# Optimization experiments

Hardware: AMD Instinct MI355X
Metric: run time of the kernel (lower is better)

The kernel has to match this reference:

```python
import jax, jax.numpy as jnp
import numpy as np

EPS_NORM = 1e-6  # MVLayerNorm epsilon


def _build_cayley():
    # Cl(3,0): blades as bitmasks, ordered by (grade, bitmask):
    # [1, e1, e2, e3, e12, e13, e23, e123]
    n = 3
    order = sorted(range(1 << n), key=lambda b: (bin(b).count('1'), b))
    idx = {b: i for i, b in enumerate(order)}
    C = np.zeros((8, 8, 8), dtype=np.float32)
    for a in range(8):
        for b in range(8):
            # sign from reordering basis vectors (Euclidean metric: e_i^2 = +1)
            swaps, ash = 0, a >> 1
            while ash:
                swaps += bin(ash & b).count('1')
                ash >>= 1
            C[idx[a], idx[a ^ b], idx[b]] = -1.0 if swaps % 2 else 1.0
    return C

_CAYLEY_NP = _build_cayley()
CAYLEY = jnp.asarray(_CAYLEY_NP)
# metric of each blade: scalar part of blade*blade -> [1,1,1,1,-1,-1,-1,-1]
METRIC = jnp.asarray(np.array([_CAYLEY_NP[i, 0, i] for i in range(8)], dtype=np.float32))
# blade -> grade subspace index, subspace dims [1,3,3,1]
BLADE2SUB = np.array([0, 1, 1, 1, 2, 2, 2, 3])


def mv_linear(x, w, b):
    # x: (B, in, 8); w: (out, in, 4); b: (out,) added to scalar blade only
    wb = w[:, :, BLADE2SUB]                      # (out, in, 8) per-blade weight
    y = jnp.einsum('bmi,nmi->bni', x, wb)        # (B, out, 8)
    return y.at[..., 0].add(b)


def mv_layernorm(x, a):
    # quadratic form per channel: q = sum_i g_i * x_i^2, shape (B, C, 1)
    q = jnp.einsum('bci,i,bci->bc', x, METRIC, x)[..., None]
    norm = (q * q + 1e-16) ** 0.25               # smooth sqrt(|q|)
    norm = norm.mean(axis=1, keepdims=True) + EPS_NORM  # (B, 1, 1)
    return a[None, :, None] * x / norm


def setup_inputs() -> dict:
    key = jax.random.key(0)
    ks = jax.random.split(key, 8)
    N, C_IN, C_HID, NSUB = 4096, 512, 512, 4
    s = 1.0 / np.sqrt(C_IN)
    return {
        'x': jax.random.normal(ks[0], (N, C_IN, 8), jnp.float32),
        'w1': jax.random.normal(ks[1], (C_HID, C_IN, NSUB), jnp.float32) * s,
        'b1': jax.random.normal(ks[2], (C_HID,), jnp.float32) * 0.02,
        'w2': jax.random.normal(ks[3], (C_HID, C_IN, NSUB), jnp.float32) * s,
        'b2': jax.random.normal(ks[4], (C_HID,), jnp.float32) * 0.02,
        'w3': jax.random.normal(ks[5], (C_IN, C_HID, NSUB), jnp.float32) * s,
        'b3': jax.random.normal(ks[6], (C_IN,), jnp.float32) * 0.02,
        'a_norm': jax.random.normal(ks[7], (C_IN,), jnp.float32) * 0.1 + 1.0,
    }


def reference(x, w1, b1, w2, b2, w3, b3, a_norm):
    x_l = mv_linear(x, w1, b1)                       # (N, hid, 8)
    x_r = mv_linear(x, w2, b2)                       # (N, hid, 8)
    gp = jnp.einsum('bni,ijk,bnk->bnj', x_l, CAYLEY, x_r)  # sparse Cayley product
    y = mv_linear(gp, w3, b3)                        # (N, in, 8)
    return mv_layernorm(y, a_norm)
```

## Files before the change

kernel.cpp:

```cpp
#include <hip/hip_runtime.h>
#include <hip/hip_bf16.h>
#include <cstdint>
#include <cstddef>

typedef __bf16 bf16;
typedef __bf16 bf16x2_t __attribute__((ext_vector_type(2)));
typedef __bf16 bf16x4_t __attribute__((ext_vector_type(4)));
typedef __bf16 bf16x8_t __attribute__((ext_vector_type(8)));
typedef float  f32x2_t  __attribute__((ext_vector_type(2)));
typedef float  f32x4_t  __attribute__((ext_vector_type(4)));

#define NTOK 4096
#define CH   512
#define SLICE (NTOK*CH)
#define WSLICE (CH*CH)

#define AS1 __attribute__((address_space(1)))
#define AS3 __attribute__((address_space(3)))

__device__ __forceinline__ void gl_lds16(const void* g, void* l) {
    __builtin_amdgcn_global_load_lds((const AS1 unsigned int*)g,
                                     (AS3 unsigned int*)l, 16, 0, 0);
}

__global__ __launch_bounds__(256) void k_convert_x(const float* __restrict__ x,
                                                   bf16* __restrict__ xb) {
    int p = blockIdx.x * 256 + threadIdx.x;
    const f32x4_t* x4 = (const f32x4_t*)x;
    f32x4_t v0 = x4[2*p];
    f32x4_t v1 = x4[2*p+1];
    xb[0*SLICE + p] = (bf16)v0.x;
    xb[1*SLICE + p] = (bf16)v0.y;
    xb[2*SLICE + p] = (bf16)v0.z;
    xb[3*SLICE + p] = (bf16)v0.w;
    xb[4*SLICE + p] = (bf16)v1.x;
    xb[5*SLICE + p] = (bf16)v1.y;
    xb[6*SLICE + p] = (bf16)v1.z;
    xb[7*SLICE + p] = (bf16)v1.w;
}

__global__ __launch_bounds__(256) void k_convert_w(const float* __restrict__ w1,
                                                   const float* __restrict__ w2,
                                                   const float* __restrict__ w3,
                                                   bf16* __restrict__ w1b,
                                                   bf16* __restrict__ w2b,
                                                   bf16* __restrict__ w3b) {
    int p = blockIdx.x * 256 + threadIdx.x;
    const float* w = (blockIdx.y == 0) ? w1 : (blockIdx.y == 1) ? w2 : w3;
    bf16* wb       = (blockIdx.y == 0) ? w1b : (blockIdx.y == 1) ? w2b : w3b;
    f32x4_t v = ((const f32x4_t*)w)[p];
    wb[0*WSLICE + p] = (bf16)v.x;
    wb[1*WSLICE + p] = (bf16)v.y;
    wb[2*WSLICE + p] = (bf16)v.z;
    wb[3*WSLICE + p] = (bf16)v.w;
}

__global__ __launch_bounds__(512, 2) void k_gemm12(const bf16* __restrict__ xb,
                                                   const bf16* __restrict__ w1b,
                                                   const bf16* __restrict__ w2b,
                                                   bf16* __restrict__ xl,
                                                   bf16* __restrict__ xr) {
    const int blade = blockIdx.z;
    const int sub = (blade == 0) ? 0 : (blade < 4) ? 1 : (blade < 7) ? 2 : 3;
    const bf16* A  = xb  + (size_t)blade * SLICE;
    const bf16* B1 = w1b + (size_t)sub * WSLICE;
    const bf16* B2 = w2b + (size_t)sub * WSLICE;
    const int tm = blockIdx.x * 256, tn = blockIdx.y * 128;

    __shared__ __align__(1024) bf16 lsA[2][256 * 64];
    __shared__ __align__(1024) bf16 lsB1[2][128 * 64];
    __shared__ __align__(1024) bf16 lsB2[2][128 * 64];

    const int t = threadIdx.x, lane = t & 63, wid = t >> 6;
    const int waveM = (wid >> 2) * 128, waveN = (wid & 3) * 32;

    const int srow = t >> 3;
    const int sswz = ((t & 7) ^ (srow & 7)) * 8;
    const bf16* Ag  = A  + (size_t)(tm + srow) * CH + sswz;
    const bf16* B1g = B1 + (size_t)(tn + srow) * CH + sswz;
    const bf16* B2g = B2 + (size_t)(tn + srow) * CH + sswz;
    const int wbase = wid * 1024;

    const int xorv  = (lane & 7) << 4;
    const int kbase = (lane >> 4) * 16;

    f32x4_t accL[8][2] = {};
    f32x4_t accR[8][2] = {};

    {
        char* la  = (char*)lsA[0]  + wbase;
        char* lb1 = (char*)lsB1[0] + wbase;
        char* lb2 = (char*)lsB2[0] + wbase;
        #pragma unroll
        for (int q = 0; q < 4; ++q)
            gl_lds16(Ag + (size_t)q * 64 * CH, la + q * 8192);
        #pragma unroll
        for (int q = 0; q < 2; ++q) {
            gl_lds16(B1g + (size_t)q * 64 * CH, lb1 + q * 8192);
            gl_lds16(B2g + (size_t)q * 64 * CH, lb2 + q * 8192);
        }
    }

    #pragma unroll 2
    for (int kt = 0; kt < 8; ++kt) {
        const int cur = kt & 1;
        __syncthreads();
        if (kt < 7) {
            const int k0 = (kt + 1) * 64;
            char* la  = (char*)lsA[cur ^ 1]  + wbase;
            char* lb1 = (char*)lsB1[cur ^ 1] + wbase;
            char* lb2 = (char*)lsB2[cur ^ 1] + wbase;
            #pragma unroll
            for (int q = 0; q < 4; ++q)
                gl_lds16(Ag + (size_t)q * 64 * CH + k0, la + q * 8192);
            #pragma unroll
            for (int q = 0; q < 2; ++q) {
                gl_lds16(B1g + (size_t)q * 64 * CH + k0, lb1 + q * 8192);
                gl_lds16(B2g + (size_t)q * 64 * CH + k0, lb2 + q * 8192);
            }
        }
        const char* ca  = (const char*)lsA[cur];
        const char* cb1 = (const char*)lsB1[cur];
        const char* cb2 = (const char*)lsB2[cur];
        #pragma unroll
        for (int kk = 0; kk < 2; ++kk) {
            const int koff = kk * 64 + kbase;
            bf16x8_t af[8], b1f[2], b2f[2];
            #pragma unroll
            for (int mf = 0; mf < 8; ++mf) {
                int row = waveM + mf * 16 + (lane & 15);
                af[mf] = *(const bf16x8_t*)(ca + row * 128 + (koff ^ xorv));
            }
            #pragma unroll
            for (int nf = 0; nf < 2; ++nf) {
                int row = waveN + nf * 16 + (lane & 15);
                b1f[nf] = *(const bf16x8_t*)(cb1 + row * 128 + (koff ^ xorv));
                b2f[nf] = *(const bf16x8_t*)(cb2 + row * 128 + (koff ^ xorv));
            }
            __builtin_amdgcn_s_setprio(1);
            #pragma unroll
            for (int mf = 0; mf < 8; ++mf)
                #pragma unroll
                for (int nf = 0; nf < 2; ++nf) {
                    accL[mf][nf] = __builtin_amdgcn_mfma_f32_16x16x32_bf16(
                        af[mf], b1f[nf], accL[mf][nf], 0, 0, 0);
                    accR[mf][nf] = __builtin_amdgcn_mfma_f32_16x16x32_bf16(
                        af[mf], b2f[nf], accR[mf][nf], 0, 0, 0);
                }
            __builtin_amdgcn_s_setprio(0);
        }
    }

    bf16* O1 = xl + (size_t)blade * SLICE;
    bf16* O2 = xr + (size_t)blade * SLICE;
    const int orow0 = tm + waveM + (lane >> 4) * 4;
    const int ocol  = tn + waveN + (lane & 15);
    #pragma unroll
    for (int mf = 0; mf < 8; ++mf)
        #pragma unroll
        for (int r = 0; r < 4; ++r) {
            size_t rowoff = (size_t)(orow0 + mf * 16 + r) * CH;
            #pragma unroll
            for (int nf = 0; nf < 2; ++nf) {
                O1[rowoff + ocol + nf * 16] = (bf16)accL[mf][nf][r];
                O2[rowoff + ocol + nf * 16] = (bf16)accR[mf][nf][r];
            }
        }
}

__global__ __launch_bounds__(512, 2) void k_gemm3(const bf16* __restrict__ gp,
                                                  const bf16* __restrict__ w3b,
                                                  bf16* __restrict__ yb) {
    const int blade = blockIdx.z;
    const int sub = (blade == 0) ? 0 : (blade < 4) ? 1 : (blade < 7) ? 2 : 3;
    const bf16* A = gp  + (size_t)blade * SLICE;
    const bf16* B = w3b + (size_t)sub * WSLICE;
    const int tm = blockIdx.x * 256, tn = blockIdx.y * 256;

    __shared__ __align__(1024) bf16 lsA[2][256 * 64];
    __shared__ __align__(1024) bf16 lsB[2][256 * 64];

    const int t = threadIdx.x, lane = t & 63, wid = t >> 6;
    const int waveM = (wid >> 2) * 128, waveN = (wid & 3) * 64;

    const int srow = t >> 3;
    const int sswz = ((t & 7) ^ (srow & 7)) * 8;
    const bf16* Ag = A + (size_t)(tm + srow) * CH + sswz;
    const bf16* Bg = B + (size_t)(tn + srow) * CH + sswz;
    const int wbase = wid * 1024;

    const int xorv  = (lane & 7) << 4;
    const int kbase = (lane >> 4) * 16;

    f32x4_t acc[8][4] = {};

    {
        char* la = (char*)lsA[0] + wbase;
        char* lb = (char*)lsB[0] + wbase;
        #pragma unroll
        for (int q = 0; q < 4; ++q) {
            gl_lds16(Ag + (size_t)q * 64 * CH, la + q * 8192);
            gl_lds16(Bg + (size_t)q * 64 * CH, lb + q * 8192);
        }
    }

    #pragma unroll 2
    for (int kt = 0; kt < 8; ++kt) {
        const int cur = kt & 1;
        __syncthreads();
        if (kt < 7) {
            const int k0 = (kt + 1) * 64;
            char* la = (char*)lsA[cur ^ 1] + wbase;
            char* lb = (char*)lsB[cur ^ 1] + wbase;
            #pragma unroll
            for (int q = 0; q < 4; ++q) {
                gl_lds16(Ag + (size_t)q * 64 * CH + k0, la + q * 8192);
                gl_lds16(Bg + (size_t)q * 64 * CH + k0, lb + q * 8192);
            }
        }
        const char* ca = (const char*)lsA[cur];
        const char* cb = (const char*)lsB[cur];
        #pragma unroll
        for (int kk = 0; kk < 2; ++kk) {
            const int koff = kk * 64 + kbase;
            bf16x8_t af[8], bf[4];
            #pragma unroll
            for (int mf = 0; mf < 8; ++mf) {
                int row = waveM + mf * 16 + (lane & 15);
                af[mf] = *(const bf16x8_t*)(ca + row * 128 + (koff ^ xorv));
            }
            #pragma unroll
            for (int nf = 0; nf < 4; ++nf) {
                int row = waveN + nf * 16 + (lane & 15);
                bf[nf] = *(const bf16x8_t*)(cb + row * 128 + (koff ^ xorv));
            }
            __builtin_amdgcn_s_setprio(1);
            #pragma unroll
            for (int mf = 0; mf < 8; ++mf)
                #pragma unroll
                for (int nf = 0; nf < 4; ++nf)
                    acc[mf][nf] = __builtin_amdgcn_mfma_f32_16x16x32_bf16(
                        af[mf], bf[nf], acc[mf][nf], 0, 0, 0);
            __builtin_amdgcn_s_setprio(0);
        }
    }

    bf16* O = yb + (size_t)blade * SLICE;
    const int orow0 = tm + waveM + (lane >> 4) * 4;
    const int ocol  = tn + waveN + (lane & 15);
    #pragma unroll
    for (int mf = 0; mf < 8; ++mf)
        #pragma unroll
        for (int r = 0; r < 4; ++r) {
            size_t rowoff = (size_t)(orow0 + mf * 16 + r) * CH;
            #pragma unroll
            for (int nf = 0; nf < 4; ++nf)
                O[rowoff + ocol + nf * 16] = (bf16)acc[mf][nf][r];
        }
}

__global__ __launch_bounds__(256) void k_gp(const bf16* __restrict__ xl,
                                            const bf16* __restrict__ xr,
                                            const float* __restrict__ b1,
                                            const float* __restrict__ b2,
                                            bf16* __restrict__ gp) {
    int p = (blockIdx.x * 256 + threadIdx.x) * 4;
    float l[8][4], r[8][4], g[8][4];
    #pragma unroll
    for (int i = 0; i < 8; ++i) {
        bf16x4_t lv = *(const bf16x4_t*)(xl + (size_t)i * SLICE + p);
        bf16x4_t rv = *(const bf16x4_t*)(xr + (size_t)i * SLICE + p);
        #pragma unroll
        for (int v = 0; v < 4; ++v) { l[i][v] = (float)lv[v]; r[i][v] = (float)rv[v]; g[i][v] = 0.f; }
    }
    int n0 = p & (CH - 1);
    f32x4_t b1v = *(const f32x4_t*)(b1 + n0);
    f32x4_t b2v = *(const f32x4_t*)(b2 + n0);
    #pragma unroll
    for (int v = 0; v < 4; ++v) { l[0][v] += b1v[v]; r[0][v] += b2v[v]; }

    const int IDX[8] = {0, 1, 2, 4, 3, 5, 6, 7};
    #pragma unroll
    for (int a = 0; a < 8; ++a) {
        #pragma unroll
        for (int b = 0; b < 8; ++b) {
            int e = ((((a >> 1) ^ (a >> 2)) & b) & 1) ^ (((a >> 2) & (b >> 1)) & 1);
            int j = IDX[a ^ b], ia = IDX[a], ib = IDX[b];
            #pragma unroll
            for (int v = 0; v < 4; ++v)
                g[j][v] += e ? (-l[ia][v] * r[ib][v]) : (l[ia][v] * r[ib][v]);
        }
    }
    #pragma unroll
    for (int i = 0; i < 8; ++i) {
        bf16x4_t gv;
        #pragma unroll
        for (int v = 0; v < 4; ++v) gv[v] = (bf16)g[i][v];
        *(bf16x4_t*)(gp + (size_t)i * SLICE + p) = gv;
    }
}

__global__ __launch_bounds__(256) void k_ln(const bf16* __restrict__ y,
                                            const float* __restrict__ b3,
                                            const float* __restrict__ an,
                                            float* __restrict__ out) {
    int b = blockIdx.x, t = threadIdx.x;
    int c0 = t * 2;
    size_t base = (size_t)b * CH + c0;
    float yv[2][8];
    #pragma unroll
    for (int i = 0; i < 8; ++i) {
        bf16x2_t v = *(const bf16x2_t*)(y + (size_t)i * SLICE + base);
        yv[0][i] = (float)v[0];
        yv[1][i] = (float)v[1];
    }
    f32x2_t b3v = *(const f32x2_t*)(b3 + c0);
    float nsum = 0.f;
    #pragma unroll
    for (int h = 0; h < 2; ++h) {
        yv[h][0] += b3v[h];
        float q = yv[h][0]*yv[h][0] + yv[h][1]*yv[h][1] + yv[h][2]*yv[h][2] + yv[h][3]*yv[h][3]
                - yv[h][4]*yv[h][4] - yv[h][5]*yv[h][5] - yv[h][6]*yv[h][6] - yv[h][7]*yv[h][7];
        nsum += sqrtf(sqrtf(q * q + 1e-16f));
    }
    #pragma unroll
    for (int off = 32; off; off >>= 1) nsum += __shfl_xor(nsum, off);
    __shared__ float red[4];
    if ((t & 63) == 0) red[t >> 6] = nsum;
    __syncthreads();
    float denom = (red[0] + red[1] + red[2] + red[3]) * (1.f / 512.f) + 1e-6f;
    float inv = 1.f / denom;
    f32x2_t anv = *(const f32x2_t*)(an + c0);
    float out16[16];
    #pragma unroll
    for (int h = 0; h < 2; ++h) {
        float s = anv[h] * inv;
        #pragma unroll
        for (int i = 0; i < 8; ++i) out16[h * 8 + i] = yv[h][i] * s;
    }
    size_t base8 = base * 8;
    #pragma unroll
    for (int j = 0; j < 4; ++j)
        *(f32x4_t*)(out + base8 + j * 4) = *(f32x4_t*)(out16 + j * 4);
}

extern "C" void kernel_launch(void* const* d_in, const int* in_sizes, int n_in,
                              void* d_out, int out_size, void* d_ws, size_t ws_size,
                              hipStream_t stream) {
    (void)in_sizes; (void)n_in; (void)out_size; (void)ws_size;
    const float* x  = (const float*)d_in[0];
    const float* w1 = (const float*)d_in[1];
    const float* b1 = (const float*)d_in[2];
    const float* w2 = (const float*)d_in[3];
    const float* b2 = (const float*)d_in[4];
    const float* w3 = (const float*)d_in[5];
    const float* b3 = (const float*)d_in[6];
    const float* an = (const float*)d_in[7];

    char* ws = (char*)d_ws;
    bf16*  xb  = (bf16*)(ws);
    bf16*  xl  = (bf16*)(ws + 33554432);
    bf16*  xr  = (bf16*)(ws + 67108864);
    bf16*  yb  = (bf16*)(ws + 33554432);
    bf16*  w1b = (bf16*)(ws + 100663296);
    bf16*  w2b = (bf16*)(ws + 102760448);
    bf16*  w3b = (bf16*)(ws + 104857600);

    k_convert_x<<<SLICE / 256, 256, 0, stream>>>(x, xb);
    dim3 gw(WSLICE / 256, 3);
    k_convert_w<<<gw, 256, 0, stream>>>(w1, w2, w3, w1b, w2b, w3b);

    dim3 g12(NTOK / 256, CH / 128, 8);
    k_gemm12<<<g12, 512, 0, stream>>>(xb, w1b, w2b, xl, xr);
    k_gp<<<SLICE / 4 / 256, 256, 0, stream>>>(xl, xr, b1, b2, xb );
    dim3 g3(NTOK / 256, CH / 256, 8);
    k_gemm3<<<g3, 512, 0, stream>>>(xb, w3b, yb);
    k_ln<<<NTOK, 256, 0, stream>>>(yb, b3, an, (float*)d_out);
}
```

Baseline: 246.4 us.

## Prefetch two K-tiles ahead with explicit waitcnt barriers and vectorized epilogue stores

```diff
diff --git a/kernel.cpp b/kernel.cpp
--- a/kernel.cpp
+++ b/kernel.cpp
@@ -22,6 +22,10 @@
     __builtin_amdgcn_global_load_lds((const AS1 unsigned int*)g,
                                      (AS3 unsigned int*)l, 16, 0, 0);
 }
+
+#define VM_WAIT(N) asm volatile("s_waitcnt vmcnt(" #N ")" ::: "memory")
+#define SFENCE()   __builtin_amdgcn_sched_barrier(0)
+#define RAW_BAR()  { SFENCE(); __builtin_amdgcn_s_barrier(); SFENCE(); }
 
 __global__ __launch_bounds__(256) void k_convert_x(const float* __restrict__ x,
                                                    bf16* __restrict__ xb) {
@@ -87,38 +91,30 @@
     f32x4_t accL[8][2] = {};
     f32x4_t accR[8][2] = {};
 
-    {
-        char* la  = (char*)lsA[0]  + wbase;
-        char* lb1 = (char*)lsB1[0] + wbase;
-        char* lb2 = (char*)lsB2[0] + wbase;
-        #pragma unroll
-        for (int q = 0; q < 4; ++q)
-            gl_lds16(Ag + (size_t)q * 64 * CH, la + q * 8192);
-        #pragma unroll
-        for (int q = 0; q < 2; ++q) {
-            gl_lds16(B1g + (size_t)q * 64 * CH, lb1 + q * 8192);
-            gl_lds16(B2g + (size_t)q * 64 * CH, lb2 + q * 8192);
-        }
-    }
+    #define STAGE12(buf, k0) {                                              \
+        char* la_  = (char*)lsA[buf]  + wbase;                              \
+        char* lb1_ = (char*)lsB1[buf] + wbase;                              \
+        char* lb2_ = (char*)lsB2[buf] + wbase;                              \
+        _Pragma("unroll")                                                   \
+        for (int q = 0; q < 4; ++q)                                         \
+            gl_lds16(Ag + (size_t)q * 64 * CH + (k0), la_ + q * 8192);      \
+        _Pragma("unroll")                                                   \
+        for (int q = 0; q < 2; ++q) {                                       \
+            gl_lds16(B1g + (size_t)q * 64 * CH + (k0), lb1_ + q * 8192);    \
+            gl_lds16(B2g + (size_t)q * 64 * CH + (k0), lb2_ + q * 8192);    \
+        }                                                                   \
+    }
+
+    STAGE12(0, 0);
+    SFENCE();
+    STAGE12(1, 64);
+    SFENCE();
+    VM_WAIT(8);
+    RAW_BAR();
 
     #pragma unroll 2
     for (int kt = 0; kt < 8; ++kt) {
         const int cur = kt & 1;
-        __syncthreads();
-        if (kt < 7) {
-            const int k0 = (kt + 1) * 64;
-            char* la  = (char*)lsA[cur ^ 1]  + wbase;
-            char* lb1 = (char*)lsB1[cur ^ 1] + wbase;
-            char* lb2 = (char*)lsB2[cur ^ 1] + wbase;
-            #pragma unroll
-            for (int q = 0; q < 4; ++q)
-                gl_lds16(Ag + (size_t)q * 64 * CH + k0, la + q * 8192);
-            #pragma unroll
-            for (int q = 0; q < 2; ++q) {
-                gl_lds16(B1g + (size_t)q * 64 * CH + k0, lb1 + q * 8192);
-                gl_lds16(B2g + (size_t)q * 64 * CH + k0, lb2 + q * 8192);
-            }
-        }
         const char* ca  = (const char*)lsA[cur];
         const char* cb1 = (const char*)lsB1[cur];
         const char* cb2 = (const char*)lsB2[cur];
@@ -143,29 +139,45 @@
                 #pragma unroll
                 for (int nf = 0; nf < 2; ++nf) {
                     accL[mf][nf] = __builtin_amdgcn_mfma_f32_16x16x32_bf16(
-                        af[mf], b1f[nf], accL[mf][nf], 0, 0, 0);
+                        b1f[nf], af[mf], accL[mf][nf], 0, 0, 0);
                     accR[mf][nf] = __builtin_amdgcn_mfma_f32_16x16x32_bf16(
-                        af[mf], b2f[nf], accR[mf][nf], 0, 0, 0);
+                        b2f[nf], af[mf], accR[mf][nf], 0, 0, 0);
                 }
             __builtin_amdgcn_s_setprio(0);
-        }
-    }
+            SFENCE();
+        }
+        RAW_BAR();
+        if (kt < 6) {
+            STAGE12(cur, (kt + 2) * 64);
+            SFENCE();
+            VM_WAIT(8);
+            RAW_BAR();
+        } else if (kt == 6) {
+            VM_WAIT(0);
+            RAW_BAR();
+        }
+    }
+    #undef STAGE12
 
     bf16* O1 = xl + (size_t)blade * SLICE;
     bf16* O2 = xr + (size_t)blade * SLICE;
-    const int orow0 = tm + waveM + (lane >> 4) * 4;
-    const int ocol  = tn + waveN + (lane & 15);
-    #pragma unroll
-    for (int mf = 0; mf < 8; ++mf)
-        #pragma unroll
-        for (int r = 0; r < 4; ++r) {
-            size_t rowoff = (size_t)(orow0 + mf * 16 + r) * CH;
-            #pragma unroll
-            for (int nf = 0; nf < 2; ++nf) {
-                O1[rowoff + ocol + nf * 16] = (bf16)accL[mf][nf][r];
-                O2[rowoff + ocol + nf * 16] = (bf16)accR[mf][nf][r];
+    const int ob  = tm + waveM + (lane & 15);
+    const int on0 = tn + waveN + (lane >> 4) * 4;
+    #pragma unroll
+    for (int mf = 0; mf < 8; ++mf) {
+        size_t rowoff = (size_t)(ob + mf * 16) * CH;
+        #pragma unroll
+        for (int nf = 0; nf < 2; ++nf) {
+            bf16x4_t v1, v2;
+            #pragma unroll
+            for (int r = 0; r < 4; ++r) {
+                v1[r] = (bf16)accL[mf][nf][r];
+                v2[r] = (bf16)accR[mf][nf][r];
             }
-        }
+            *(bf16x4_t*)(O1 + rowoff + on0 + nf * 16) = v1;
+            *(bf16x4_t*)(O2 + rowoff + on0 + nf * 16) = v2;
+        }
+    }
 }
 
 __global__ __launch_bounds__(512, 2) void k_gemm3(const bf16* __restrict__ gp,
@@ -194,30 +206,26 @@
 
     f32x4_t acc[8][4] = {};
 
-    {
-        char* la = (char*)lsA[0] + wbase;
-        char* lb = (char*)lsB[0] + wbase;
-        #pragma unroll
-        for (int q = 0; q < 4; ++q) {
-            gl_lds16(Ag + (size_t)q * 64 * CH, la + q * 8192);
-            gl_lds16(Bg + (size_t)q * 64 * CH, lb + q * 8192);
-        }
-    }
+    #define STAGE3(buf, k0) {                                               \
+        char* la_ = (char*)lsA[buf] + wbase;                                \
+        char* lb_ = (char*)lsB[buf] + wbase;                                \
+        _Pragma("unroll")                                                   \
+        for (int q = 0; q < 4; ++q) {                                       \
+            gl_lds16(Ag + (size_t)q * 64 * CH + (k0), la_ + q * 8192);      \
+            gl_lds16(Bg + (size_t)q * 64 * CH + (k0), lb_ + q * 8192);      \
+        }                                                                   \
+    }
+
+    STAGE3(0, 0);
+    SFENCE();
+    STAGE3(1, 64);
+    SFENCE();
+    VM_WAIT(8);
+    RAW_BAR();
 
     #pragma unroll 2
     for (int kt = 0; kt < 8; ++kt) {
         const int cur = kt & 1;
-        __syncthreads();
-        if (kt < 7) {
-            const int k0 = (kt + 1) * 64;
-            char* la = (char*)lsA[cur ^ 1] + wbase;
-            char* lb = (char*)lsB[cur ^ 1] + wbase;
-            #pragma unroll
-            for (int q = 0; q < 4; ++q) {
-                gl_lds16(Ag + (size_t)q * 64 * CH + k0, la + q * 8192);
-                gl_lds16(Bg + (size_t)q * 64 * CH + k0, lb + q * 8192);
-            }
-        }
         const char* ca = (const char*)lsA[cur];
         const char* cb = (const char*)lsB[cur];
         #pragma unroll
@@ -240,23 +248,37 @@
                 #pragma unroll
                 for (int nf = 0; nf < 4; ++nf)
                     acc[mf][nf] = __builtin_amdgcn_mfma_f32_16x16x32_bf16(
-                        af[mf], bf[nf], acc[mf][nf], 0, 0, 0);
+                        bf[nf], af[mf], acc[mf][nf], 0, 0, 0);
             __builtin_amdgcn_s_setprio(0);
-        }
-    }
+            SFENCE();
+        }
+        RAW_BAR();
+        if (kt < 6) {
+            STAGE3(cur, (kt + 2) * 64);
+            SFENCE();
+            VM_WAIT(8);
+            RAW_BAR();
+        } else if (kt == 6) {
+            VM_WAIT(0);
+            RAW_BAR();
+        }
+    }
+    #undef STAGE3
 
     bf16* O = yb + (size_t)blade * SLICE;
-    const int orow0 = tm + waveM + (lane >> 4) * 4;
-    const int ocol  = tn + waveN + (lane & 15);
-    #pragma unroll
-    for (int mf = 0; mf < 8; ++mf)
-        #pragma unroll
-        for (int r = 0; r < 4; ++r) {
-            size_t rowoff = (size_t)(orow0 + mf * 16 + r) * CH;
-            #pragma unroll
-            for (int nf = 0; nf < 4; ++nf)
-                O[rowoff + ocol + nf * 16] = (bf16)acc[mf][nf][r];
-        }
+    const int ob  = tm + waveM + (lane & 15);
+    const int on0 = tn + waveN + (lane >> 4) * 4;
+    #pragma unroll
+    for (int mf = 0; mf < 8; ++mf) {
+        size_t rowoff = (size_t)(ob + mf * 16) * CH;
+        #pragma unroll
+        for (int nf = 0; nf < 4; ++nf) {
+            bf16x4_t v;
+            #pragma unroll
+            for (int r = 0; r < 4; ++r) v[r] = (bf16)acc[mf][nf][r];
+            *(bf16x4_t*)(O + rowoff + on0 + nf * 16) = v;
+        }
+    }
 }
 
 __global__ __launch_bounds__(256) void k_gp(const bf16* __restrict__ xl,
```

Result: slower. 255.0 us (+3.5%).
